# Performance work log

Measured on AMD Instinct MI355X. Metric: run time of the kernel, lower is better.

The kernel has to match this reference:

```python
import jax, jax.numpy as jnp
import numpy as np

KH, KW = 5, 5
STRIDE = 1


def _extract_patches(x, kh, kw, s):
    """x: (B,C,H,W) -> (B, oh*ow, C*kh*kw), flattened in (C,kh,kw) row-major order
    to match torch's window.reshape(B, -1)."""
    B, C, H, W = x.shape
    oh = (H - kh) // s + 1
    ow = (W - kw) // s + 1
    i = (jnp.arange(oh) * s)[:, None] + jnp.arange(kh)[None, :]      # (oh, kh)
    j = (jnp.arange(ow) * s)[:, None] + jnp.arange(kw)[None, :]      # (ow, kw)
    # fancy-index -> (B, C, oh, kh, ow, kw)
    p = x[:, :, i[:, :, None, None], j[None, None, :, :]]
    p = p.transpose(0, 2, 4, 1, 3, 5)                                # (B, oh, ow, C, kh, kw)
    return p.reshape(B, oh * ow, C * kh * kw), oh, ow


def _cdist(a, w):
    """a: (B,P,D), w: (O,D) -> Euclidean distance (B,P,O)."""
    a2 = jnp.sum(a * a, axis=-1, keepdims=True)          # (B,P,1)
    w2 = jnp.sum(w * w, axis=-1)                         # (O,)
    d2 = a2 + w2[None, None, :] - 2.0 * jnp.einsum('bpd,od->bpo', a, w)
    return jnp.sqrt(jnp.maximum(d2, 0.0))


def setup_inputs() -> dict:
    key = jax.random.key(0)
    k1, k2, k3, k4 = jax.random.split(key, 4)
    B, O = 32, 64
    H = W = 112
    gray_input = jax.random.normal(k1, (B, 1, H, W), dtype=jnp.float32)
    rgb_input = jax.random.normal(k2, (B, 1, H, W), dtype=jnp.float32)
    # kaiming-uniform-like init, first filter zeroed as in reset_parameters
    bound = 1.0 / np.sqrt(KH * KW)
    gray_weight = jax.random.uniform(k3, (O, 1, KH, KW), jnp.float32, -bound, bound)
    gray_weight = gray_weight.at[0].set(0.0)
    rgb_weight = jax.random.uniform(k4, (O, 1, KH, KW), jnp.float32, -bound, bound)
    rgb_weight = rgb_weight.at[0].set(0.0)
    std = jnp.full((1,), 2.0, dtype=jnp.float32)
    return {"gray_input": gray_input, "rgb_input": rgb_input,
            "gray_weight": gray_weight, "rgb_weight": rgb_weight, "std": std}


def reference(gray_input, rgb_input, gray_weight, rgb_weight, std):
    B = gray_input.shape[0]
    O = gray_weight.shape[0]
    gp, oh, ow = _extract_patches(gray_input, KH, KW, STRIDE)   # (B,P,D)
    rp, _, _ = _extract_patches(rgb_input, KH, KW, STRIDE)      # (B,P,D)
    gw = gray_weight.reshape(O, -1)                             # (O,D)
    rw = rgb_weight.reshape(O, -1)                              # (O,D)
    dist = _cdist(gp, gw) + _cdist(rp, rw)                      # (B,P,O)
    s = std[0]
    rbf = jnp.exp(-(dist * dist) / (2.0 * s * s))               # gaussian RBF
    return rbf.transpose(0, 2, 1).reshape(B, O, oh, ow)
```

## Files before the change

kernel.cpp:

```cpp
#include <hip/hip_runtime.h>

constexpr int KH = 5, KW = 5;
constexpr int O  = 64;
constexpr int D  = KH * KW;
constexpr int H  = 112, W = 112;
constexpr int OH = H - KH + 1;
constexpr int OW = W - KW + 1;
constexpr int P  = OH * OW;

typedef __attribute__((ext_vector_type(8))) short short8v;
typedef __attribute__((ext_vector_type(4))) float float4v;

constexpr int    WF_SHORTS = 4 * 2 * 2 * 64 * 8;
constexpr size_t WS_BYTES  = WF_SHORTS * sizeof(short);

__global__ void prep_weights_mfma(const float* __restrict__ gw,
                                  const float* __restrict__ rw,
                                  void* wsv) {
    short* wfrag = (short*)wsv;
    const int t = threadIdx.x;
    for (int u = t; u < 1024; u += 256) {
        const int lane = u & 63;
        const int cfg  = u >> 6;
        const int sp   = cfg & 1;
        const int img  = (cfg >> 1) & 1;
        const int Mt   = cfg >> 2;
        const int hi   = lane >> 4, c = lane & 15;
        const float* wt = img ? rw : gw;
        const int o = Mt * 16 + c;
        short8v v;
        #pragma unroll
        for (int j = 0; j < 8; ++j) {
            const int k = hi * 8 + j;
            float w;
            if (k < D) {
                w = wt[o * D + k];
            } else if (k == D) {
                float s2 = 0.f;
                for (int kk = 0; kk < D; ++kk) {
                    float x = wt[o * D + kk];
                    s2 = fmaf(x, x, s2);
                }
                w = -0.5f * s2;
            } else {
                w = 0.f;
            }
            const unsigned bits = __float_as_uint(w);
            if (sp == 0) {
                v[j] = (short)(bits >> 16);
            } else {
                const float hf = __uint_as_float(bits & 0xFFFF0000u);
                v[j] = (short)(__float_as_uint(w - hf) >> 16);
            }
        }
        *(short8v*)(wfrag + (cfg * 64 + lane) * 8) = v;
    }
}

__global__ __launch_bounds__(256, 3) void rbf_mfma(
    const float* __restrict__ gin, const float* __restrict__ rin,
    const void* __restrict__ wsv,  const float* __restrict__ stdp,
    float* __restrict__ out)
{
    const short* wfrag = (const short*)wsv;
    const int lane = threadIdx.x & 63;
    const int hi   = lane >> 4;
    const int c    = lane & 15;
    const int wid  = blockIdx.x * 4 + (threadIdx.x >> 6);
    const int tile0 = wid * 8;

    short8v wf[4][2][2];
    #pragma unroll
    for (int Mt = 0; Mt < 4; ++Mt)
        #pragma unroll
        for (int img = 0; img < 2; ++img)
            #pragma unroll
            for (int sp = 0; sp < 2; ++sp)
                wf[Mt][img][sp] = *(const short8v*)(wfrag +
                    (((Mt * 2 + img) * 2 + sp) * 64 + lane) * 8);

    int offs[8];
    #pragma unroll
    for (int j = 0; j < 8; ++j) {
        const int k  = hi * 8 + j;
        const int ki = k / 5, kj = k - ki * 5;
        offs[j] = (k < D) ? (ki * W + kj) : 0;
    }

    const float s  = stdp[0];
    const float k2 = -1.442695040888963f / (2.f * s * s);

    auto addr = [&](int t, const float*& gb, const float*& rb, float*& ob) {
        const unsigned pg0 = (unsigned)(tile0 + t) * 16u;
        const unsigned b   = pg0 / (unsigned)P;
        const unsigned p0  = pg0 - b * (unsigned)P;
        const unsigned p   = p0 + (unsigned)c;
        const unsigned y   = p / (unsigned)OW;
        const unsigned x   = p - y * (unsigned)OW;
        const int ibase = (int)((b * H + y) * W + x);
        gb = gin + ibase;
        rb = rin + ibase;
        ob = out + (size_t)b * O * P + p0 + c;
    };

    auto load8 = [&](float (&v)[8], const float* base) {
        #pragma unroll
        for (int j = 0; j < 8; ++j) v[j] = base[offs[j]];
    };

    auto split_one = [&](const float (&v)[8], short8v& ph, short8v& pl, float& a2o) {
        float full = 0.f;
        #pragma unroll
        for (int j = 0; j < 8; ++j) full = fmaf(v[j], v[j], full);
        float part = (hi == 3) ? v[0] * v[0] : full;
        part += __shfl_xor(part, 16);
        part += __shfl_xor(part, 32);
        a2o = part;
        #pragma unroll
        for (int j = 0; j < 8; ++j) {
            const unsigned bits = __float_as_uint(v[j]);
            const float hf = __uint_as_float(bits & 0xFFFF0000u);
            ph[j] = (short)(bits >> 16);
            pl[j] = (short)(__float_as_uint(v[j] - hf) >> 16);
        }
        if (hi == 3) { ph[1] = (short)0x3F80; pl[1] = (short)0; }
    };

    auto process = [&](float (&vg)[8], float (&vr)[8], float* ob) {
        short8v pf[2][2];
        float a2v[2];
        split_one(vg, pf[0][0], pf[0][1], a2v[0]);
        split_one(vr, pf[1][0], pf[1][1], a2v[1]);

        const float4v z4 = {0.f, 0.f, 0.f, 0.f};
        float4v acc[4][2];
        #pragma unroll
        for (int Mt = 0; Mt < 4; ++Mt) {
            #pragma unroll
            for (int img = 0; img < 2; ++img) {
                float4v a0 = __builtin_amdgcn_mfma_f32_16x16x32_bf16(
                    wf[Mt][img][0], pf[img][0], z4, 0, 0, 0);
                a0 = __builtin_amdgcn_mfma_f32_16x16x32_bf16(
                    wf[Mt][img][1], pf[img][0], a0, 0, 0, 0);
                acc[Mt][img] = __builtin_amdgcn_mfma_f32_16x16x32_bf16(
                    wf[Mt][img][0], pf[img][1], a0, 0, 0, 0);
            }
        }

        #pragma unroll
        for (int Mt = 0; Mt < 4; ++Mt) {
            #pragma unroll
            for (int reg = 0; reg < 4; ++reg) {
                float dg = fmaxf(fmaf(-2.f, acc[Mt][0][reg], a2v[0]), 0.f);
                float dr = fmaxf(fmaf(-2.f, acc[Mt][1][reg], a2v[1]), 0.f);
                float t2 = fmaf(2.f, __builtin_amdgcn_sqrtf(dg * dr), dg + dr);
                ob[(size_t)(Mt * 16 + hi * 4 + reg) * P] =
                    __builtin_amdgcn_exp2f(k2 * t2);
            }
        }
    };

    const float *gbA, *rbA, *gbB, *rbB;
    float *obA, *obB;
    float vgA[8], vrA[8], vgB[8], vrB[8];

    addr(0, gbA, rbA, obA);
    load8(vgA, gbA); load8(vrA, rbA);

    #pragma unroll 1
    for (int it = 0; it < 4; ++it) {
        addr(2 * it + 1, gbB, rbB, obB);
        load8(vgB, gbB); load8(vrB, rbB);
        process(vgA, vrA, obA);
        if (it < 3) {
            addr(2 * it + 2, gbA, rbA, obA);
            load8(vgA, gbA); load8(vrA, rbA);
        }
        process(vgB, vrB, obB);
    }
}

__global__ __launch_bounds__(256) void rbf_conv_fallback(
    const float* __restrict__ gin, const float* __restrict__ rin,
    const float* __restrict__ gw,  const float* __restrict__ rw,
    const float* __restrict__ stdp, float* __restrict__ out, int B)
{
    __shared__ float s_w2g[O], s_w2r[O];
    const int t = threadIdx.x;
    if (t < O) {
        float sg = 0.f, sr = 0.f;
        #pragma unroll
        for (int k = 0; k < D; ++k) {
            float a = gw[t * D + k]; sg = fmaf(a, a, sg);
            float b = rw[t * D + k]; sr = fmaf(b, b, sr);
        }
        s_w2g[t] = sg;
        s_w2r[t] = sr;
    }
    __syncthreads();

    const int idx = blockIdx.x * blockDim.x + t;
    if (idx >= B * P) return;
    const int b = idx / P;
    const int p = idx - b * P;
    const int y = p / OW;
    const int x = p - y * OW;

    const float* gb = gin + (b * H + y) * W + x;
    const float* rb = rin + (b * H + y) * W + x;
    float ga[D], ra[D];
    float a2g = 0.f, a2r = 0.f;
    #pragma unroll
    for (int i = 0; i < KH; ++i)
        #pragma unroll
        for (int j = 0; j < KW; ++j) {
            float g = gb[i * W + j]; ga[i * KW + j] = g; a2g = fmaf(g, g, a2g);
            float r = rb[i * W + j]; ra[i * KW + j] = r; a2r = fmaf(r, r, a2r);
        }

    const float s    = stdp[0];
    const float ninv = -1.0f / (2.0f * s * s);
    float* ob = out + (size_t)b * O * P + p;

    for (int o = 0; o < O; ++o) {
        float dg = 0.f, dr = 0.f;
        #pragma unroll
        for (int k = 0; k < D; ++k) {
            dg = fmaf(ga[k], gw[o * D + k], dg);
            dr = fmaf(ra[k], rw[o * D + k], dr);
        }
        float d2g = fmaxf(a2g + s_w2g[o] - 2.0f * dg, 0.f);
        float d2r = fmaxf(a2r + s_w2r[o] - 2.0f * dr, 0.f);
        float dist = __fsqrt_rn(d2g) + __fsqrt_rn(d2r);
        ob[(size_t)o * P] = __expf(ninv * dist * dist);
    }
}

extern "C" void kernel_launch(void* const* d_in, const int* in_sizes, int n_in,
                              void* d_out, int out_size, void* d_ws, size_t ws_size,
                              hipStream_t stream) {
    const float* gin  = (const float*)d_in[0];
    const float* rin  = (const float*)d_in[1];
    const float* gw   = (const float*)d_in[2];
    const float* rw   = (const float*)d_in[3];
    const float* stdp = (const float*)d_in[4];
    float* out = (float*)d_out;

    const int B = in_sizes[0] / (H * W);

    const int totalTiles = B * P / 16;
    if (ws_size >= WS_BYTES && d_ws != nullptr &&
        (B * P) % 16 == 0 && totalTiles % 8 == 0) {
        prep_weights_mfma<<<1, 256, 0, stream>>>(gw, rw, d_ws);
        const int waves  = totalTiles / 8;
        const int blocks = (waves + 3) / 4;
        rbf_mfma<<<blocks, 256, 0, stream>>>(gin, rin, d_ws, stdp, out);
    } else {
        const int total = B * P;
        const int block = 256;
        const int grid  = (total + block - 1) / block;
        rbf_conv_fallback<<<grid, block, 0, stream>>>(gin, rin, gw, rw, stdp, out, B);
    }
}
```

Before: 34.98 us.

## Move low-half weight fragments to LDS, halve tiles per wave, drop software pipelining

```diff
diff --git a/kernel.cpp b/kernel.cpp
--- a/kernel.cpp
+++ b/kernel.cpp
@@ -7,28 +7,26 @@
 constexpr int OH = H - KH + 1;
 constexpr int OW = W - KW + 1;
 constexpr int P  = OH * OW;
+constexpr int TPW = 4;
 
 typedef __attribute__((ext_vector_type(8))) short short8v;
 typedef __attribute__((ext_vector_type(4))) float float4v;
-
-constexpr int    WF_SHORTS = 4 * 2 * 2 * 64 * 8;
-constexpr size_t WS_BYTES  = WF_SHORTS * sizeof(short);
+typedef __attribute__((ext_vector_type(4))) unsigned int uint4v;
+
+constexpr size_t WS_BYTES = 8192 * sizeof(short);
 
 __global__ void prep_weights_mfma(const float* __restrict__ gw,
                                   const float* __restrict__ rw,
                                   void* wsv) {
-    short* wfrag = (short*)wsv;
+    short* ws = (short*)wsv;
     const int t = threadIdx.x;
-    for (int u = t; u < 1024; u += 256) {
-        const int lane = u & 63;
-        const int cfg  = u >> 6;
-        const int sp   = cfg & 1;
-        const int img  = (cfg >> 1) & 1;
-        const int Mt   = cfg >> 2;
-        const int hi   = lane >> 4, c = lane & 15;
+    for (int u = t; u < 512; u += 256) {
+        const int lane = u & 63, mi = u >> 6;
+        const int img = mi & 1, Mt = mi >> 1;
+        const int hi = lane >> 4, c = lane & 15;
         const float* wt = img ? rw : gw;
         const int o = Mt * 16 + c;
-        short8v v;
+        short vh[8], vl[8];
         #pragma unroll
         for (int j = 0; j < 8; ++j) {
             const int k = hi * 8 + j;
@@ -46,38 +44,47 @@
                 w = 0.f;
             }
             const unsigned bits = __float_as_uint(w);
-            if (sp == 0) {
-                v[j] = (short)(bits >> 16);
-            } else {
-                const float hf = __uint_as_float(bits & 0xFFFF0000u);
-                v[j] = (short)(__float_as_uint(w - hf) >> 16);
-            }
-        }
-        *(short8v*)(wfrag + (cfg * 64 + lane) * 8) = v;
-    }
-}
-
-__global__ __launch_bounds__(256, 3) void rbf_mfma(
+            const float hf = __uint_as_float(bits & 0xFFFF0000u);
+            vh[j] = (short)(bits >> 16);
+            vl[j] = (short)(__float_as_uint(w - hf) >> 16);
+        }
+        short* dh = ws + (mi * 64 + lane) * 8;
+        short* dl = dh + 4096;
+        #pragma unroll
+        for (int j = 0; j < 8; ++j) { dh[j] = vh[j]; dl[j] = vl[j]; }
+    }
+}
+
+__device__ inline unsigned pack_hi2(float a, float b) {
+    return __builtin_amdgcn_perm(__float_as_uint(b), __float_as_uint(a),
+                                 0x07060302u);
+}
+
+__global__ __launch_bounds__(256, 4) void rbf_mfma(
     const float* __restrict__ gin, const float* __restrict__ rin,
     const void* __restrict__ wsv,  const float* __restrict__ stdp,
     float* __restrict__ out)
 {
     const short* wfrag = (const short*)wsv;
+    __shared__ short wlo_s[4096];
+
+    {
+        const short* wlo_g = wfrag + 4096;
+        for (int i = threadIdx.x; i < 512; i += 256)
+            *(uint4v*)(wlo_s + i * 8) = *(const uint4v*)(wlo_g + i * 8);
+    }
+
     const int lane = threadIdx.x & 63;
     const int hi   = lane >> 4;
     const int c    = lane & 15;
+    const bool hi3 = (hi == 3);
     const int wid  = blockIdx.x * 4 + (threadIdx.x >> 6);
-    const int tile0 = wid * 8;
-
-    short8v wf[4][2][2];
+    const int tile0 = wid * TPW;
+
+    short8v wh[8];
     #pragma unroll
-    for (int Mt = 0; Mt < 4; ++Mt)
-        #pragma unroll
-        for (int img = 0; img < 2; ++img)
-            #pragma unroll
-            for (int sp = 0; sp < 2; ++sp)
-                wf[Mt][img][sp] = *(const short8v*)(wfrag +
-                    (((Mt * 2 + img) * 2 + sp) * 64 + lane) * 8);
+    for (int mi = 0; mi < 8; ++mi)
+        wh[mi] = *(const short8v*)(wfrag + (mi * 64 + lane) * 8);
 
     int offs[8];
     #pragma unroll
@@ -90,7 +97,10 @@
     const float s  = stdp[0];
     const float k2 = -1.442695040888963f / (2.f * s * s);
 
-    auto addr = [&](int t, const float*& gb, const float*& rb, float*& ob) {
+    __syncthreads();
+
+    #pragma unroll 1
+    for (int t = 0; t < TPW; ++t) {
         const unsigned pg0 = (unsigned)(tile0 + t) * 16u;
         const unsigned b   = pg0 / (unsigned)P;
         const unsigned p0  = pg0 - b * (unsigned)P;
@@ -98,39 +108,42 @@
         const unsigned y   = p / (unsigned)OW;
         const unsigned x   = p - y * (unsigned)OW;
         const int ibase = (int)((b * H + y) * W + x);
-        gb = gin + ibase;
-        rb = rin + ibase;
-        ob = out + (size_t)b * O * P + p0 + c;
-    };
-
-    auto load8 = [&](float (&v)[8], const float* base) {
-        #pragma unroll
-        for (int j = 0; j < 8; ++j) v[j] = base[offs[j]];
-    };
-
-    auto split_one = [&](const float (&v)[8], short8v& ph, short8v& pl, float& a2o) {
-        float full = 0.f;
-        #pragma unroll
-        for (int j = 0; j < 8; ++j) full = fmaf(v[j], v[j], full);
-        float part = (hi == 3) ? v[0] * v[0] : full;
-        part += __shfl_xor(part, 16);
-        part += __shfl_xor(part, 32);
-        a2o = part;
-        #pragma unroll
-        for (int j = 0; j < 8; ++j) {
-            const unsigned bits = __float_as_uint(v[j]);
-            const float hf = __uint_as_float(bits & 0xFFFF0000u);
-            ph[j] = (short)(bits >> 16);
-            pl[j] = (short)(__float_as_uint(v[j] - hf) >> 16);
-        }
-        if (hi == 3) { ph[1] = (short)0x3F80; pl[1] = (short)0; }
-    };
-
-    auto process = [&](float (&vg)[8], float (&vr)[8], float* ob) {
-        short8v pf[2][2];
+        const float* gb = gin + ibase;
+        const float* rb = rin + ibase;
+
+        short8v pfh[2], pfl[2];
         float a2v[2];
-        split_one(vg, pf[0][0], pf[0][1], a2v[0]);
-        split_one(vr, pf[1][0], pf[1][1], a2v[1]);
+        #pragma unroll
+        for (int img = 0; img < 2; ++img) {
+            const float* base = img ? rb : gb;
+            float v[8];
+            #pragma unroll
+            for (int j = 0; j < 8; ++j) v[j] = base[offs[j]];
+
+            float full = 0.f;
+            #pragma unroll
+            for (int j = 0; j < 8; ++j) full = fmaf(v[j], v[j], full);
+            float part = hi3 ? v[0] * v[0] : full;
+            part += __shfl_xor(part, 16);
+            part += __shfl_xor(part, 32);
+            a2v[img] = part;
+
+            float lf[8];
+            #pragma unroll
+            for (int j = 0; j < 8; ++j) {
+                const float hf = __uint_as_float(__float_as_uint(v[j]) & 0xFFFF0000u);
+                lf[j] = v[j] - hf;
+            }
+            uint4v uh, ul;
+            uh.x = pack_hi2(v[0], v[1]);  uh.y = pack_hi2(v[2], v[3]);
+            uh.z = pack_hi2(v[4], v[5]);  uh.w = pack_hi2(v[6], v[7]);
+            ul.x = pack_hi2(lf[0], lf[1]); ul.y = pack_hi2(lf[2], lf[3]);
+            ul.z = pack_hi2(lf[4], lf[5]); ul.w = pack_hi2(lf[6], lf[7]);
+            uh.x = hi3 ? ((uh.x & 0x0000FFFFu) | 0x3F800000u) : uh.x;
+            ul.x = hi3 ? (ul.x & 0x0000FFFFu) : ul.x;
+            pfh[img] = __builtin_bit_cast(short8v, uh);
+            pfl[img] = __builtin_bit_cast(short8v, ul);
+        }
 
         const float4v z4 = {0.f, 0.f, 0.f, 0.f};
         float4v acc[4][2];
@@ -138,15 +151,18 @@
         for (int Mt = 0; Mt < 4; ++Mt) {
             #pragma unroll
             for (int img = 0; img < 2; ++img) {
+                const int mi = Mt * 2 + img;
                 float4v a0 = __builtin_amdgcn_mfma_f32_16x16x32_bf16(
-                    wf[Mt][img][0], pf[img][0], z4, 0, 0, 0);
+                    wh[mi], pfh[img], z4, 0, 0, 0);
+                const short8v wl = *(const short8v*)(wlo_s + (mi * 64 + lane) * 8);
                 a0 = __builtin_amdgcn_mfma_f32_16x16x32_bf16(
-                    wf[Mt][img][1], pf[img][0], a0, 0, 0, 0);
+                    wl, pfh[img], a0, 0, 0, 0);
                 acc[Mt][img] = __builtin_amdgcn_mfma_f32_16x16x32_bf16(
-                    wf[Mt][img][0], pf[img][1], a0, 0, 0, 0);
-            }
-        }
-
+                    wh[mi], pfl[img], a0, 0, 0, 0);
+            }
+        }
+
+        float* obh = out + (size_t)b * O * P + p0 + c + (size_t)hi * 4 * P;
         #pragma unroll
         for (int Mt = 0; Mt < 4; ++Mt) {
             #pragma unroll
@@ -154,29 +170,9 @@
                 float dg = fmaxf(fmaf(-2.f, acc[Mt][0][reg], a2v[0]), 0.f);
                 float dr = fmaxf(fmaf(-2.f, acc[Mt][1][reg], a2v[1]), 0.f);
                 float t2 = fmaf(2.f, __builtin_amdgcn_sqrtf(dg * dr), dg + dr);
-                ob[(size_t)(Mt * 16 + hi * 4 + reg) * P] =
-                    __builtin_amdgcn_exp2f(k2 * t2);
-            }
-        }
-    };
-
-    const float *gbA, *rbA, *gbB, *rbB;
-    float *obA, *obB;
-    float vgA[8], vrA[8], vgB[8], vrB[8];
-
-    addr(0, gbA, rbA, obA);
-    load8(vgA, gbA); load8(vrA, rbA);
-
-    #pragma unroll 1
-    for (int it = 0; it < 4; ++it) {
-        addr(2 * it + 1, gbB, rbB, obB);
-        load8(vgB, gbB); load8(vrB, rbB);
-        process(vgA, vrA, obA);
-        if (it < 3) {
-            addr(2 * it + 2, gbA, rbA, obA);
-            load8(vgA, gbA); load8(vrA, rbA);
-        }
-        process(vgB, vrB, obB);
+                obh[(size_t)(Mt * 16 + reg) * P] = __builtin_amdgcn_exp2f(k2 * t2);
+            }
+        }
     }
 }
 
@@ -247,12 +243,12 @@
     float* out = (float*)d_out;
 
     const int B = in_sizes[0] / (H * W);
-
     const int totalTiles = B * P / 16;
+
     if (ws_size >= WS_BYTES && d_ws != nullptr &&
-        (B * P) % 16 == 0 && totalTiles % 8 == 0) {
+        (B * P) % 16 == 0 && totalTiles % TPW == 0) {
         prep_weights_mfma<<<1, 256, 0, stream>>>(gw, rw, d_ws);
-        const int waves  = totalTiles / 8;
+        const int waves  = totalTiles / TPW;
         const int blocks = (waves + 3) / 4;
         rbf_mfma<<<blocks, 256, 0, stream>>>(gin, rin, d_ws, stdp, out);
     } else {
```

After: 48.39 us. 1.38x slower.
